# Optimization experiments

Hardware: AMD Instinct MI355X
Metric: run time of the kernel (lower is better)

## Reference

```python
import jax, jax.numpy as jnp
import numpy as np

CN = 64  # cn_base

def conv2d(x, w, b):
    y = jax.lax.conv_general_dilated(x, w, (1, 1), 'SAME', dimension_numbers=('NCHW', 'OIHW', 'NCHW'))
    return y + b[None, :, None, None]

def epipolar_unfold(feat, xy, bw):
    # feat [B,C,h,w], xy [B,np,el,2] int (x,y) -> [B,C,(2bw+1)*el,np]
    B, C, h, w = feat.shape
    npx, el = xy.shape[1], xy.shape[2]
    dy = jnp.arange(-bw, bw + 1)                                   # band offsets [K]
    y = jnp.clip(xy[..., 1][..., None] + dy, 0, h - 1)             # [B,np,el,K]
    x = jnp.clip(xy[..., 0], 0, w - 1)[..., None]                  # [B,np,el,1]
    idx = (y * w + x).reshape(B, -1)                               # [B,np*el*K]
    out = jnp.take_along_axis(feat.reshape(B, C, h * w), idx[:, None, :], axis=2)
    out = out.reshape(B, C, npx, el * (2 * bw + 1))
    return jnp.transpose(out, (0, 1, 3, 2))                        # [B,C,nsz,np]

def setup_inputs():
    key = jax.random.key(0)
    ks = jax.random.split(key, 20)
    b, ns, c, h, w, el, D, bw = 1, 4, 3, 64, 64, 8, 8, 1
    npx = h * w
    nsz = (2 * bw + 1) * el
    cn_emb = (ns - 1) * 2 + 3 * CN + 2 + 6  # 206
    rn = lambda i, shp, s=1.0: jax.random.normal(ks[i], shp, jnp.float32) * s
    return {
        'source_views': rn(0, (b, ns, c, h, w)),
        'source_flows': rn(1, (b, ns, ns - 1, 2, h, w)),
        'psvs': rn(2, (b, ns, c, D, h, w)),
        'warped_source_views': rn(3, (b, ns, ns - 1, c, h, w)),
        'source_posemaps': rn(4, (b, ns, 6)),
        'neighbor_xy': jax.random.randint(ks[5], (b, ns, npx, el, 2), 0, w, jnp.int32),
        'spa_code': rn(6, (b, ns, 2, nsz, npx)),
        'ang_code': rn(7, (b, ns, 6, nsz, npx)),
        'band_width': bw,
        'flow_w': rn(8, (CN, (ns - 1) * 2 + c + (ns - 1) * c, 3, 3), 0.02),
        'flow_b': rn(9, (CN,), 0.02),
        'ctx_w': rn(10, (CN, c, 3, 3), 0.02),
        'ctx_b': rn(11, (CN,), 0.02),
        'wnet_w': rn(12, (cn_emb, 1), 0.02),
        'wnet_b': rn(13, (1,), 0.02),
        'cnet_w': rn(14, (cn_emb, 1), 0.02),
        'cnet_b': rn(15, (1,), 0.02),
        'psv_w': rn(16, (CN, 2 * c, 3, 3), 0.02),
        'psv_b': rn(17, (CN,), 0.02),
        'vref_w': rn(18, (c, c + 2 * ns * CN, 3, 3), 0.02),
        'vref_b': rn(19, (c,), 0.02),
    }

def reference(source_views, source_flows, psvs, warped_source_views, source_posemaps,
              neighbor_xy, spa_code, ang_code, band_width,
              flow_w, flow_b, ctx_w, ctx_b, wnet_w, wnet_b, cnet_w, cnet_b,
              psv_w, psv_b, vref_w, vref_b):
    b, ns, c, h, w = source_views.shape
    npx, el = neighbor_xy.shape[2], neighbor_xy.shape[3]
    ps = int(round(npx ** 0.5))
    D = psvs.shape[3]
    bw = int(band_width)
    nsz = (2 * bw + 1) * el
    B = b * ns
    sv = source_views.reshape(B, c, h, w)
    sf = source_flows.reshape(B, (ns - 1) * 2, h, w)
    wv = warped_source_views.reshape(B, (ns - 1) * c, h, w)
    nxy = neighbor_xy.reshape(B, npx, el, 2)
    spa = spa_code.reshape(B, 2, nsz, npx)
    ang = ang_code.reshape(B, 6, nsz, npx)
    # sub-networks (flowRefNet / ctxNet)
    ce = jax.nn.relu(conv2d(jnp.concatenate([sf, sv, wv], axis=1), flow_w, flow_b))  # [B,64,h,w]
    ctx = jax.nn.relu(conv2d(sv, ctx_w, ctx_b))                                      # [B,64,h,w]
    # epipolar gathers -> [B,C,nsz,np]
    sv_u = epipolar_unfold(sv, nxy, bw)
    ctx_u = epipolar_unfold(ctx, nxy, bw)
    ce_u = epipolar_unfold(ce, nxy, bw)
    sf_u = epipolar_unfold(sf, nxy, bw)
    mu = jnp.broadcast_to(jnp.mean(ce_u, axis=2, keepdims=True), ce_u.shape)
    var = jnp.broadcast_to(jnp.var(ce_u, axis=2, keepdims=True, ddof=1), ce_u.shape)
    emb = jnp.concatenate([sf_u, ce_u, mu, var, spa, ang], axis=1)   # [B,206,nsz,np]
    # weightNet: per-pixel softmax weight over neighbor_size
    emb_t = jnp.transpose(emb, (0, 3, 2, 1))                          # [B,np,nsz,206]
    weight = jax.nn.softmax((emb_t @ wnet_w)[..., 0] + wnet_b[0], axis=-1)  # [B,np,nsz]
    w_sg = jax.lax.stop_gradient(weight)
    interp_view = jnp.einsum('bcnp,bpn->bpc', sv_u, weight)           # [B,np,c]
    interp_ctx = jnp.einsum('bknp,bpn->bpk', ctx_u, w_sg)             # [B,np,64]
    interp_emb = jnp.einsum('bknp,bpn->bpk', emb, w_sg)               # [B,np,206]
    # confNet: softmax confidence over sources
    ie = jnp.transpose(interp_emb.reshape(b, ns, npx, -1), (0, 2, 1, 3))  # [b,np,ns,206]
    confs = jax.nn.softmax((ie @ cnet_w)[..., 0] + cnet_b[0], axis=2)     # [b,np,ns]
    iv4 = interp_view.reshape(b, ns, npx, c)
    blended = jnp.einsum('bspc,bps->bpc', iv4, confs)                 # [b,np,c]
    blended_img = jnp.transpose(blended, (0, 2, 1)).reshape(b, c, ps, ps)
    # psvNet: per depth-slice conv then mean over D
    psv_sl = jnp.transpose(psvs, (0, 1, 3, 2, 4, 5)).reshape(b * ns * D, c, ps, ps)
    bexp = jnp.broadcast_to(blended_img[:, None, None], (b, ns, D, c, ps, ps)).reshape(b * ns * D, c, ps, ps)
    psv_feat = jax.nn.relu(conv2d(jnp.concatenate([psv_sl, bexp], axis=1), psv_w, psv_b))
    psv_feat = psv_feat.reshape(b, ns, D, CN, ps, ps).mean(axis=2)    # [b,ns,64,ps,ps]
    ictx = jnp.transpose(interp_ctx.reshape(b, ns, ps, ps, CN), (0, 1, 4, 2, 3)).reshape(b, ns * CN, ps, ps)
    ref_in = jnp.concatenate([blended_img, ictx, psv_feat.reshape(b, ns * CN, ps, ps)], axis=1)
    ref_novel_view = conv2d(ref_in, vref_w, vref_b)                   # [b,3,ps,ps]
    return (ref_novel_view,
            blended_img,
            jnp.transpose(interp_view.reshape(b, ns, ps, ps, c), (0, 1, 4, 2, 3)),
            weight.reshape(b, ns, ps, ps, nsz),
            jnp.transpose(confs, (0, 2, 1)).reshape(b, ns, ps, ps))
```

## Files before the change

### kernel.cpp

```cpp
#include <hip/hip_runtime.h>
#include <hip/hip_bf16.h>


#define NS   4
#define NPX  4096
#define NSZ  24
#define PS   64
#define VINW 520
#define HW   34

#define OFF0 0
#define OFF1 12288
#define OFF2 24576
#define OFF3 73728
#define OFF4 466944

__device__ unsigned g_cc [NS * NPX * 64];
__device__ float2 g_fld[NS * NPX];
__device__ float2 g_sa [NS * NPX * NSZ];
__device__ __align__(16) unsigned short g_vin [NPX * VINW];
__device__ float g_iv  [NS * NPX * 3];
__device__ float g_clg [NS * NPX];
__device__ float g_fwT [162 * 64];
__device__ float g_cwT [27 * 64];
__device__ float g_pwT [54 * 64];
__device__ __align__(16) unsigned short g_vwT [3 * 9 * VINW];

__device__ __forceinline__ int clampi(int v, int lo, int hi) {
    return v < lo ? lo : (v > hi ? hi : v);
}
__device__ __forceinline__ unsigned bf16_bits(float f) {
    unsigned u = __float_as_uint(f);
    return (u + 0x7fffu + ((u >> 16) & 1u)) >> 16;
}
__device__ __forceinline__ float bf16_lo(unsigned v) { return __uint_as_float(v << 16); }
__device__ __forceinline__ float bf16_hi(unsigned v) { return __uint_as_float(v & 0xffff0000u); }
__device__ __forceinline__ float ldbf(const unsigned short* p, int i) {
    return __uint_as_float(((unsigned)p[i]) << 16);
}

__global__ __launch_bounds__(256) void k_prep(
    const float* __restrict__ fw, const float* __restrict__ cw,
    const float* __restrict__ pw, const float* __restrict__ vw,
    const float* __restrict__ spa, const float* __restrict__ ang,
    const float* __restrict__ ww, const float* __restrict__ cnw)
{
    const int i = blockIdx.x * 256 + threadIdx.x;
    const int stride = gridDim.x * 256;
    for (int d = i; d < 162 * 64; d += stride) g_fwT[d] = fw[(d & 63) * 162 + (d >> 6)];
    for (int d = i; d < 27 * 64;  d += stride) g_cwT[d] = cw[(d & 63) * 27  + (d >> 6)];
    for (int d = i; d < 54 * 64;  d += stride) g_pwT[d] = pw[(d & 63) * 54  + (d >> 6)];
    for (int d = i; d < 3 * 9 * VINW; d += stride) {
        const int oc = d / (9 * VINW), rem = d % (9 * VINW);
        const int t = rem / VINW, nch = rem % VINW;
        float v = 0.f;
        if (nch < 256)      v = vw[(oc * 515 + 3 + nch) * 9 + t];
        else if (nch < 512) v = vw[(oc * 515 + 259 + (nch - 256)) * 9 + t];
        else if (nch < 515) v = vw[(oc * 515 + (nch - 512)) * 9 + t];
        g_vwT[d] = (unsigned short)bf16_bits(v);
    }

    {
        const int s = i >> 12, p = i & 4095;
        float2 acc[NSZ];
        #pragma unroll
        for (int n = 0; n < NSZ; ++n) acc[n] = make_float2(0.f, 0.f);
        #pragma unroll
        for (int c = 0; c < 2; ++c) {
            const float a = ww[198 + c], b = cnw[198 + c];
            #pragma unroll
            for (int n = 0; n < NSZ; ++n) {
                const float v = spa[((s * 2 + c) * NSZ + n) * NPX + p];
                acc[n].x += v * a;
                acc[n].y += v * b;
            }
        }
        #pragma unroll
        for (int c = 0; c < 6; ++c) {
            const float a = ww[200 + c], b = cnw[200 + c];
            #pragma unroll
            for (int n = 0; n < NSZ; ++n) {
                const float v = ang[((s * 6 + c) * NSZ + n) * NPX + p];
                acc[n].x += v * a;
                acc[n].y += v * b;
            }
        }
        float2* dst = g_sa + (size_t)(s * NPX + p) * NSZ;
        #pragma unroll
        for (int n = 0; n < NSZ; ++n) dst[n] = acc[n];
    }
}

__global__ __launch_bounds__(256) void k_convs(
    const float* __restrict__ sv, const float* __restrict__ sf, const float* __restrict__ wv,
    const float* __restrict__ flow_b, const float* __restrict__ ctx_b,
    const float* __restrict__ wnet_w, const float* __restrict__ cnet_w)
{
    __shared__ float lds[18 * 3 * HW];
    const int blk = blockIdx.x;
    const int s = blk >> 7, py = (blk & 127) >> 1, half = blk & 1;
    const int tid = threadIdx.x;

    for (int i = tid; i < 18 * 3 * HW; i += 256) {
        const int lc = i % HW;
        const int rr = (i / HW) % 3;
        const int pl = i / (3 * HW);
        const int iy = py + rr - 1;
        const int ix = half * 32 + lc - 1;
        float v = 0.f;
        if ((unsigned)iy < 64u && (unsigned)ix < 64u) {
            const float* src = (pl < 6) ? (sf + (s * 6 + pl) * NPX)
                             : (pl < 9) ? (sv + (s * 3 + (pl - 6)) * NPX)
                                        : (wv + (s * 9 + (pl - 9)) * NPX);
            v = src[iy * 64 + ix];
        }
        lds[i] = v;
    }
    __syncthreads();

    const int oc  = tid & 63;
    const int wid = tid >> 6;
    const int lc0 = wid * 8;

    float acc_ce[8], acc_ctx[8];
    const float fb = flow_b[oc], cb = ctx_b[oc];
    #pragma unroll
    for (int j = 0; j < 8; ++j) { acc_ce[j] = fb; acc_ctx[j] = cb; }

    for (int pl = 0; pl < 18; ++pl) {
        float w[9];
        #pragma unroll
        for (int t = 0; t < 9; ++t) w[t] = g_fwT[(pl * 9 + t) * 64 + oc];
        float wc[9];
        const bool has_ctx = (pl >= 6 && pl < 9);
        if (has_ctx) {
            #pragma unroll
            for (int t = 0; t < 9; ++t) wc[t] = g_cwT[((pl - 6) * 9 + t) * 64 + oc];
        }
        float c0[3], c1[3], c2[3];
        #pragma unroll
        for (int r = 0; r < 3; ++r) {
            c0[r] = lds[(pl * 3 + r) * HW + lc0];
            c1[r] = lds[(pl * 3 + r) * HW + lc0 + 1];
        }
        #pragma unroll
        for (int j = 0; j < 8; ++j) {
            #pragma unroll
            for (int r = 0; r < 3; ++r)
                c2[r] = lds[(pl * 3 + r) * HW + lc0 + j + 2];
            float a = 0.f;
            #pragma unroll
            for (int r = 0; r < 3; ++r)
                a += c0[r] * w[r * 3 + 0] + c1[r] * w[r * 3 + 1] + c2[r] * w[r * 3 + 2];
            acc_ce[j] += a;
            if (has_ctx) {
                float b2 = 0.f;
                #pragma unroll
                for (int r = 0; r < 3; ++r)
                    b2 += c0[r] * wc[r * 3 + 0] + c1[r] * wc[r * 3 + 1] + c2[r] * wc[r * 3 + 2];
                acc_ctx[j] += b2;
            }
            #pragma unroll
            for (int r = 0; r < 3; ++r) { c0[r] = c1[r]; c1[r] = c2[r]; }
        }
    }

    const float Wce = wnet_w[6 + oc], Cce = cnet_w[6 + oc];
    float awsel = 0.f, acsel = 0.f;
    #pragma unroll
    for (int j = 0; j < 8; ++j) {
        const float ce = fmaxf(acc_ce[j], 0.f);
        const float cx = fmaxf(acc_ctx[j], 0.f);
        const int p = py * 64 + half * 32 + wid * 8 + j;
        g_cc[(s * NPX + p) * 64 + oc] = bf16_bits(ce) | (bf16_bits(cx) << 16);
        float gw = ce * Wce, gc = ce * Cce;
        #pragma unroll
        for (int off = 32; off; off >>= 1) {
            gw += __shfl_xor(gw, off, 64);
            gc += __shfl_xor(gc, off, 64);
        }
        awsel = (oc == j) ? gw : awsel;
        acsel = (oc == j) ? gc : acsel;
    }
    if (oc < 8) {
        const int lpx = wid * 8 + oc;
        float fwv = 0.f, fcv = 0.f;
        #pragma unroll
        for (int c = 0; c < 6; ++c) {
            const float v = lds[(c * 3 + 1) * HW + lpx + 1];
            fwv += v * wnet_w[c];
            fcv += v * cnet_w[c];
        }
        g_fld[s * NPX + py * 64 + half * 32 + lpx] = make_float2(awsel + fwv, acsel + fcv);
    }
}

__global__ __launch_bounds__(256) void k_epi(
    const float* __restrict__ sv, const int* __restrict__ nxy,
    const float* __restrict__ wnet_w, const float* __restrict__ wnet_b,
    const float* __restrict__ cnet_w,
    float* __restrict__ out)
{
    const int blk = blockIdx.x;
    const int wid = threadIdx.x >> 6;
    const int l   = threadIdx.x & 63;
    const int s   = (blk & 7) >> 1;
    const int p   = (blk >> 3) * 8 + (blk & 1) * 4 + wid;

    int q[NSZ];
    #pragma unroll
    for (int e = 0; e < 8; ++e) {
        int nx = nxy[((s * NPX + p) * 8 + e) * 2 + 0];
        int ny = nxy[((s * NPX + p) * 8 + e) * 2 + 1];
        nx = clampi(nx, 0, 63);
        #pragma unroll
        for (int k = 0; k < 3; ++k) {
            int y = clampi(ny + k - 1, 0, 63);
            q[e * 3 + k] = y * 64 + nx;
        }
    }

    const unsigned* ccp = g_cc + (size_t)s * NPX * 64;
    unsigned cc[NSZ];
    #pragma unroll
    for (int n = 0; n < NSZ; ++n) cc[n] = ccp[q[n] * 64 + l];

    float mu = 0.f;
    #pragma unroll
    for (int n = 0; n < NSZ; ++n) mu += bf16_lo(cc[n]);
    mu *= (1.f / 24.f);
    float var = 0.f;
    #pragma unroll
    for (int n = 0; n < NSZ; ++n) { const float d = bf16_lo(cc[n]) - mu; var += d * d; }
    var *= (1.f / 23.f);

    float pw = mu * wnet_w[70 + l] + var * wnet_w[134 + l];
    float pc = mu * cnet_w[70 + l] + var * cnet_w[134 + l];
    #pragma unroll
    for (int off = 32; off; off >>= 1) {
        pw += __shfl_xor(pw, off, 64);
        pc += __shfl_xor(pc, off, 64);
    }
    const float base_w = pw, base_c = pc;

    float Aw = 0.f, Ac = 0.f;
    if (l < NSZ) {
        const float2 A = g_fld[s * NPX + q[l]];
        const float2 B = g_sa[(size_t)(s * NPX + p) * NSZ + l];
        Aw = A.x + B.x; Ac = A.y + B.y;
    }

    float logit = (l < NSZ) ? (Aw + base_w + wnet_b[0]) : -1e30f;
    float mx = logit;
    #pragma unroll
    for (int off = 32; off; off >>= 1) mx = fmaxf(mx, __shfl_xor(mx, off, 64));
    float e = (l < NSZ) ? __expf(logit - mx) : 0.f;
    float ssum = e;
    #pragma unroll
    for (int off = 32; off; off >>= 1) ssum += __shfl_xor(ssum, off, 64);
    const float wgt = e / ssum;

    float clp = (l < NSZ) ? (Ac + base_c) * wgt : 0.f;
    #pragma unroll
    for (int off = 32; off; off >>= 1) clp += __shfl_xor(clp, off, 64);
    if (l == 0) g_clg[s * NPX + p] = clp;

    if (l < NSZ) out[OFF3 + (s * NPX + p) * NSZ + l] = wgt;

    float wall[NSZ];
    #pragma unroll
    for (int n = 0; n < NSZ; ++n) wall[n] = __shfl(wgt, n, 64);

    float sc = 0.f;
    #pragma unroll
    for (int n = 0; n < NSZ; ++n) sc += bf16_hi(cc[n]) * wall[n];
    g_vin[p * VINW + s * 64 + l] = (unsigned short)bf16_bits(sc);

    if (l < 3) {
        float svv = 0.f;
        #pragma unroll
        for (int n = 0; n < NSZ; ++n) svv += sv[(s * 3 + l) * NPX + q[n]] * wall[n];
        g_iv[(s * NPX + p) * 3 + l] = svv;
        out[OFF2 + (s * 3 + l) * NPX + p] = svv;
    }
}

__global__ __launch_bounds__(256) void k_psv(
    const float* __restrict__ psvs, const float* __restrict__ psv_b,
    const float* __restrict__ cnet_b, float* __restrict__ out)
{
    __shared__ float lds[27 * 3 * HW];
    const int blk = blockIdx.x;
    const int s = blk >> 7, py = (blk & 127) >> 1, half = blk & 1;
    const int tid = threadIdx.x;

    for (int i = tid; i < 27 * 3 * HW; i += 256) {
        const int lc = i % HW;
        const int rr = (i / HW) % 3;
        const int pl = i / (3 * HW);
        float v = 0.f;
        if (pl < 24) {
            const int iy = py + rr - 1;
            const int ix = half * 32 + lc - 1;
            if ((unsigned)iy < 64u && (unsigned)ix < 64u)
                v = psvs[(s * 24 + pl) * NPX + iy * 64 + ix];
        }
        lds[i] = v;
    }
    __syncthreads();

    if (tid < 3 * HW) {
        const int r = tid / HW, lc = tid % HW;
        const int iy = py + r - 1, ix = half * 32 + lc - 1;
        if ((unsigned)iy < 64u && (unsigned)ix < 64u) {
            const int p = iy * 64 + ix;
            const float cb2 = cnet_b[0];
            float lg[NS];
            #pragma unroll
            for (int ss = 0; ss < NS; ++ss) lg[ss] = g_clg[ss * NPX + p] + cb2;
            float m = lg[0];
            #pragma unroll
            for (int ss = 1; ss < NS; ++ss) m = fmaxf(m, lg[ss]);
            float ssum = 0.f;
            float conf[NS];
            #pragma unroll
            for (int ss = 0; ss < NS; ++ss) { conf[ss] = __expf(lg[ss] - m); ssum += conf[ss]; }
            const float inv = 1.f / ssum;
            #pragma unroll
            for (int ss = 0; ss < NS; ++ss) conf[ss] *= inv;
            float bl[3];
            #pragma unroll
            for (int c = 0; c < 3; ++c) {
                float a = 0.f;
                #pragma unroll
                for (int ss = 0; ss < NS; ++ss)
                    a += g_iv[(ss * NPX + p) * 3 + c] * conf[ss];
                bl[c] = a;
                lds[((24 + c) * 3 + r) * HW + lc] = a;
            }
            if (s == 0 && r == 1 && lc >= 1 && lc <= 32) {
                #pragma unroll
                for (int ss = 0; ss < NS; ++ss) out[OFF4 + ss * NPX + p] = conf[ss];
                #pragma unroll
                for (int c = 0; c < 3; ++c) {
                    out[OFF1 + c * NPX + p] = bl[c];
                    g_vin[p * VINW + 512 + c] = (unsigned short)bf16_bits(bl[c]);
                }
            }
        }
    }
    __syncthreads();

    const int oc  = tid & 63;
    const int wid = tid >> 6;
    const int lc0 = wid * 8;
    const float bias = psv_b[oc];

    float wp[3][9];
    #pragma unroll
    for (int ic = 0; ic < 3; ++ic)
        #pragma unroll
        for (int t = 0; t < 9; ++t) wp[ic][t] = g_pwT[(ic * 9 + t) * 64 + oc];

    float bconst[8];
    #pragma unroll
    for (int j = 0; j < 8; ++j) bconst[j] = bias;
    for (int ic = 0; ic < 3; ++ic) {
        float w[9];
        #pragma unroll
        for (int t = 0; t < 9; ++t) w[t] = g_pwT[((3 + ic) * 9 + t) * 64 + oc];
        const int pl = 24 + ic;
        float c0[3], c1[3], c2[3];
        #pragma unroll
        for (int r = 0; r < 3; ++r) {
            c0[r] = lds[(pl * 3 + r) * HW + lc0];
            c1[r] = lds[(pl * 3 + r) * HW + lc0 + 1];
        }
        #pragma unroll
        for (int j = 0; j < 8; ++j) {
            #pragma unroll
            for (int r = 0; r < 3; ++r)
                c2[r] = lds[(pl * 3 + r) * HW + lc0 + j + 2];
            float a = 0.f;
            #pragma unroll
            for (int r = 0; r < 3; ++r)
                a += c0[r] * w[r * 3 + 0] + c1[r] * w[r * 3 + 1] + c2[r] * w[r * 3 + 2];
            bconst[j] += a;
            #pragma unroll
            for (int r = 0; r < 3; ++r) { c0[r] = c1[r]; c1[r] = c2[r]; }
        }
    }

    float acc[8];
    #pragma unroll
    for (int j = 0; j < 8; ++j) acc[j] = 0.f;

    for (int d = 0; d < 8; ++d) {
        float a[8];
        #pragma unroll
        for (int j = 0; j < 8; ++j) a[j] = bconst[j];
        #pragma unroll
        for (int ic = 0; ic < 3; ++ic) {
            const int pl = ic * 8 + d;
            float c0[3], c1[3], c2[3];
            #pragma unroll
            for (int r = 0; r < 3; ++r) {
                c0[r] = lds[(pl * 3 + r) * HW + lc0];
                c1[r] = lds[(pl * 3 + r) * HW + lc0 + 1];
            }
            #pragma unroll
            for (int j = 0; j < 8; ++j) {
                #pragma unroll
                for (int r = 0; r < 3; ++r)
                    c2[r] = lds[(pl * 3 + r) * HW + lc0 + j + 2];
                float t2 = 0.f;
                #pragma unroll
                for (int r = 0; r < 3; ++r)
                    t2 += c0[r] * wp[ic][r * 3 + 0] + c1[r] * wp[ic][r * 3 + 1] + c2[r] * wp[ic][r * 3 + 2];
                a[j] += t2;
                #pragma unroll
                for (int r = 0; r < 3; ++r) { c0[r] = c1[r]; c1[r] = c2[r]; }
            }
        }
        #pragma unroll
        for (int j = 0; j < 8; ++j) acc[j] += fmaxf(a[j], 0.f);
    }
    #pragma unroll
    for (int j = 0; j < 8; ++j)
        g_vin[(py * 64 + half * 32 + wid * 8 + j) * VINW + 256 + s * 64 + oc] =
            (unsigned short)bf16_bits(acc[j] * 0.125f);
}

__global__ __launch_bounds__(64) void k_vref(
    const float* __restrict__ vref_b, float* __restrict__ out)
{
    const int p = blockIdx.x;
    const int py = p >> 6, px = p & 63;
    const int l = threadIdx.x;

    float acc[3] = {0.f, 0.f, 0.f};
    #pragma unroll
    for (int t = 0; t < 9; ++t) {
        const int iy = py + t / 3 - 1, ix = px + t % 3 - 1;
        if ((unsigned)iy >= 64u || (unsigned)ix >= 64u) continue;
        const int rowbase = (iy * 64 + ix) * VINW;
        const uint4 vv = *(const uint4*)(g_vin + rowbase + 8 * l);
        float v[8];
        v[0] = bf16_lo(vv.x); v[1] = bf16_hi(vv.x);
        v[2] = bf16_lo(vv.y); v[3] = bf16_hi(vv.y);
        v[4] = bf16_lo(vv.z); v[5] = bf16_hi(vv.z);
        v[6] = bf16_lo(vv.w); v[7] = bf16_hi(vv.w);
        #pragma unroll
        for (int oc = 0; oc < 3; ++oc) {
            const uint4 ww = *(const uint4*)(g_vwT + (oc * 9 + t) * VINW + 8 * l);
            acc[oc] += v[0] * bf16_lo(ww.x) + v[1] * bf16_hi(ww.x)
                     + v[2] * bf16_lo(ww.y) + v[3] * bf16_hi(ww.y)
                     + v[4] * bf16_lo(ww.z) + v[5] * bf16_hi(ww.z)
                     + v[6] * bf16_lo(ww.w) + v[7] * bf16_hi(ww.w);
        }
        if (l < 3) {
            const float bv = ldbf(g_vin, rowbase + 512 + l);
            #pragma unroll
            for (int oc = 0; oc < 3; ++oc)
                acc[oc] += bv * ldbf(g_vwT, (oc * 9 + t) * VINW + 512 + l);
        }
    }
    #pragma unroll
    for (int off = 32; off; off >>= 1) {
        #pragma unroll
        for (int oc = 0; oc < 3; ++oc)
            acc[oc] += __shfl_xor(acc[oc], off, 64);
    }
    if (l == 0) {
        #pragma unroll
        for (int oc = 0; oc < 3; ++oc)
            out[OFF0 + oc * NPX + p] = acc[oc] + vref_b[oc];
    }
}

extern "C" void kernel_launch(void* const* d_in, const int* in_sizes, int n_in,
                              void* d_out, int out_size, void* d_ws, size_t ws_size,
                              hipStream_t stream)
{
    auto find1 = [&](int sz, int fb) -> int {
        for (int i = 0; i < n_in; ++i) if (in_sizes[i] == sz) return i;
        return fb;
    };
    const int i_sv  = find1(49152, 0);
    const int i_sf  = find1(98304, 1);
    const int i_psv = find1(393216, 2);
    const int i_wv  = find1(147456, 3);
    const int i_nxy = find1(262144, 5);
    const int i_spa = find1(786432, 6);
    const int i_ang = find1(2359296, 7);
    const int i_fw  = find1(10368, 9);
    const int i_cw  = find1(1728, 11);
    const int i_pw  = find1(3456, 17);
    const int i_vw  = find1(13905, 19);
    const int i_vb  = find1(3, 20);
    int i_ww = -1, i_cnw = -1;
    for (int i = 0; i < n_in; ++i)
        if (in_sizes[i] == 206) { if (i_ww < 0) i_ww = i; else { i_cnw = i; break; } }
    if (i_ww  < 0) i_ww  = 13;
    if (i_cnw < 0) i_cnw = 15;
    int b64[3] = {10, 12, 18}; int c64 = 0;
    for (int i = 0; i < n_in && c64 < 3; ++i) if (in_sizes[i] == 64) b64[c64++] = i;
    const int i_fb = b64[0], i_cb = b64[1], i_pb = b64[2];
    int i_wb = -1, i_cnb = -1;
    for (int i = i_fw + 1; i < n_in; ++i)
        if (in_sizes[i] == 1) { if (i_wb < 0) i_wb = i; else { i_cnb = i; break; } }
    if (i_wb  < 0) i_wb  = 14;
    if (i_cnb < 0) i_cnb = 16;

    const float* sv     = (const float*)d_in[i_sv];
    const float* sf     = (const float*)d_in[i_sf];
    const float* psvs   = (const float*)d_in[i_psv];
    const float* wv     = (const float*)d_in[i_wv];
    const int*   nxy    = (const int*)d_in[i_nxy];
    const float* spa    = (const float*)d_in[i_spa];
    const float* ang    = (const float*)d_in[i_ang];
    const float* flow_w = (const float*)d_in[i_fw];
    const float* flow_b = (const float*)d_in[i_fb];
    const float* ctx_w  = (const float*)d_in[i_cw];
    const float* ctx_b  = (const float*)d_in[i_cb];
    const float* wnet_w = (const float*)d_in[i_ww];
    const float* wnet_b = (const float*)d_in[i_wb];
    const float* cnet_w = (const float*)d_in[i_cnw];
    const float* cnet_b = (const float*)d_in[i_cnb];
    const float* psv_w  = (const float*)d_in[i_pw];
    const float* psv_b  = (const float*)d_in[i_pb];
    const float* vref_w = (const float*)d_in[i_vw];
    const float* vref_b = (const float*)d_in[i_vb];
    (void)d_ws; (void)ws_size; (void)out_size;

    float* out = (float*)d_out;

    k_prep <<<64, 256, 0, stream>>>(flow_w, ctx_w, psv_w, vref_w, spa, ang, wnet_w, cnet_w);
    k_convs<<<512, 256, 0, stream>>>(sv, sf, wv, flow_b, ctx_b, wnet_w, cnet_w);
    k_epi  <<<4096, 256, 0, stream>>>(sv, nxy, wnet_w, wnet_b, cnet_w, out);
    k_psv  <<<512, 256, 0, stream>>>(psvs, psv_b, cnet_b, out);
    k_vref <<<4096, 64, 0, stream>>>(vref_b, out);
}
```

Before: 177.3 us.

## Fuse five stage kernels into one cooperative persistent kernel with grid syncs

```diff
diff --git a/kernel.cpp b/kernel.cpp
--- a/kernel.cpp
+++ b/kernel.cpp
@@ -1,5 +1,8 @@
 #include <hip/hip_runtime.h>
 #include <hip/hip_bf16.h>
+#include <hip/hip_cooperative_groups.h>
+
+namespace cg = cooperative_groups;
 
 
 #define NS   4
@@ -39,48 +42,52 @@
     return __uint_as_float(((unsigned)p[i]) << 16);
 }
 
-__global__ __launch_bounds__(256) void k_prep(
-    const float* __restrict__ fw, const float* __restrict__ cw,
-    const float* __restrict__ pw, const float* __restrict__ vw,
-    const float* __restrict__ spa, const float* __restrict__ ang,
-    const float* __restrict__ ww, const float* __restrict__ cnw)
-{
-    const int i = blockIdx.x * 256 + threadIdx.x;
-    const int stride = gridDim.x * 256;
-    for (int d = i; d < 162 * 64; d += stride) g_fwT[d] = fw[(d & 63) * 162 + (d >> 6)];
-    for (int d = i; d < 27 * 64;  d += stride) g_cwT[d] = cw[(d & 63) * 27  + (d >> 6)];
-    for (int d = i; d < 54 * 64;  d += stride) g_pwT[d] = pw[(d & 63) * 54  + (d >> 6)];
+struct Params {
+    const float *sv, *sf, *psvs, *wv;
+    const int   *nxy;
+    const float *spa, *ang;
+    const float *fw, *fb, *cw, *cb;
+    const float *ww, *wb, *cnw, *cnb;
+    const float *pw, *pb, *vw, *vb;
+    float *out;
+};
+
+
+__device__ __forceinline__ void prep_body(const Params& P, int i, int stride)
+{
+    for (int d = i; d < 162 * 64; d += stride) g_fwT[d] = P.fw[(d & 63) * 162 + (d >> 6)];
+    for (int d = i; d < 27 * 64;  d += stride) g_cwT[d] = P.cw[(d & 63) * 27  + (d >> 6)];
+    for (int d = i; d < 54 * 64;  d += stride) g_pwT[d] = P.pw[(d & 63) * 54  + (d >> 6)];
     for (int d = i; d < 3 * 9 * VINW; d += stride) {
         const int oc = d / (9 * VINW), rem = d % (9 * VINW);
         const int t = rem / VINW, nch = rem % VINW;
         float v = 0.f;
-        if (nch < 256)      v = vw[(oc * 515 + 3 + nch) * 9 + t];
-        else if (nch < 512) v = vw[(oc * 515 + 259 + (nch - 256)) * 9 + t];
-        else if (nch < 515) v = vw[(oc * 515 + (nch - 512)) * 9 + t];
+        if (nch < 256)      v = P.vw[(oc * 515 + 3 + nch) * 9 + t];
+        else if (nch < 512) v = P.vw[(oc * 515 + 259 + (nch - 256)) * 9 + t];
+        else if (nch < 515) v = P.vw[(oc * 515 + (nch - 512)) * 9 + t];
         g_vwT[d] = (unsigned short)bf16_bits(v);
     }
-
-    {
-        const int s = i >> 12, p = i & 4095;
+    for (int d = i; d < NS * NPX; d += stride) {
+        const int s = d >> 12, p = d & 4095;
         float2 acc[NSZ];
         #pragma unroll
         for (int n = 0; n < NSZ; ++n) acc[n] = make_float2(0.f, 0.f);
         #pragma unroll
         for (int c = 0; c < 2; ++c) {
-            const float a = ww[198 + c], b = cnw[198 + c];
+            const float a = P.ww[198 + c], b = P.cnw[198 + c];
             #pragma unroll
             for (int n = 0; n < NSZ; ++n) {
-                const float v = spa[((s * 2 + c) * NSZ + n) * NPX + p];
+                const float v = P.spa[((s * 2 + c) * NSZ + n) * NPX + p];
                 acc[n].x += v * a;
                 acc[n].y += v * b;
             }
         }
         #pragma unroll
         for (int c = 0; c < 6; ++c) {
-            const float a = ww[200 + c], b = cnw[200 + c];
+            const float a = P.ww[200 + c], b = P.cnw[200 + c];
             #pragma unroll
             for (int n = 0; n < NSZ; ++n) {
-                const float v = ang[((s * 6 + c) * NSZ + n) * NPX + p];
+                const float v = P.ang[((s * 6 + c) * NSZ + n) * NPX + p];
                 acc[n].x += v * a;
                 acc[n].y += v * b;
             }
@@ -91,15 +98,9 @@
     }
 }
 
-__global__ __launch_bounds__(256) void k_convs(
-    const float* __restrict__ sv, const float* __restrict__ sf, const float* __restrict__ wv,
-    const float* __restrict__ flow_b, const float* __restrict__ ctx_b,
-    const float* __restrict__ wnet_w, const float* __restrict__ cnet_w)
-{
-    __shared__ float lds[18 * 3 * HW];
-    const int blk = blockIdx.x;
-    const int s = blk >> 7, py = (blk & 127) >> 1, half = blk & 1;
-    const int tid = threadIdx.x;
+__device__ __forceinline__ void convs_body(const Params& P, float* lds, int b2, int tid)
+{
+    const int s = b2 >> 7, py = (b2 & 127) >> 1, half = b2 & 1;
 
     for (int i = tid; i < 18 * 3 * HW; i += 256) {
         const int lc = i % HW;
@@ -109,9 +110,9 @@
         const int ix = half * 32 + lc - 1;
         float v = 0.f;
         if ((unsigned)iy < 64u && (unsigned)ix < 64u) {
-            const float* src = (pl < 6) ? (sf + (s * 6 + pl) * NPX)
-                             : (pl < 9) ? (sv + (s * 3 + (pl - 6)) * NPX)
-                                        : (wv + (s * 9 + (pl - 9)) * NPX);
+            const float* src = (pl < 6) ? (P.sf + (s * 6 + pl) * NPX)
+                             : (pl < 9) ? (P.sv + (s * 3 + (pl - 6)) * NPX)
+                                        : (P.wv + (s * 9 + (pl - 9)) * NPX);
             v = src[iy * 64 + ix];
         }
         lds[i] = v;
@@ -123,7 +124,7 @@
     const int lc0 = wid * 8;
 
     float acc_ce[8], acc_ctx[8];
-    const float fb = flow_b[oc], cb = ctx_b[oc];
+    const float fb = P.fb[oc], cb = P.cb[oc];
     #pragma unroll
     for (int j = 0; j < 8; ++j) { acc_ce[j] = fb; acc_ctx[j] = cb; }
 
@@ -154,18 +155,18 @@
                 a += c0[r] * w[r * 3 + 0] + c1[r] * w[r * 3 + 1] + c2[r] * w[r * 3 + 2];
             acc_ce[j] += a;
             if (has_ctx) {
-                float b2 = 0.f;
+                float b2f = 0.f;
                 #pragma unroll
                 for (int r = 0; r < 3; ++r)
-                    b2 += c0[r] * wc[r * 3 + 0] + c1[r] * wc[r * 3 + 1] + c2[r] * wc[r * 3 + 2];
-                acc_ctx[j] += b2;
+                    b2f += c0[r] * wc[r * 3 + 0] + c1[r] * wc[r * 3 + 1] + c2[r] * wc[r * 3 + 2];
+                acc_ctx[j] += b2f;
             }
             #pragma unroll
             for (int r = 0; r < 3; ++r) { c0[r] = c1[r]; c1[r] = c2[r]; }
         }
     }
 
-    const float Wce = wnet_w[6 + oc], Cce = cnet_w[6 + oc];
+    const float Wce = P.ww[6 + oc], Cce = P.cnw[6 + oc];
     float awsel = 0.f, acsel = 0.f;
     #pragma unroll
     for (int j = 0; j < 8; ++j) {
@@ -188,30 +189,20 @@
         #pragma unroll
         for (int c = 0; c < 6; ++c) {
             const float v = lds[(c * 3 + 1) * HW + lpx + 1];
-            fwv += v * wnet_w[c];
-            fcv += v * cnet_w[c];
+            fwv += v * P.ww[c];
+            fcv += v * P.cnw[c];
         }
         g_fld[s * NPX + py * 64 + half * 32 + lpx] = make_float2(awsel + fwv, acsel + fcv);
     }
 }
 
-__global__ __launch_bounds__(256) void k_epi(
-    const float* __restrict__ sv, const int* __restrict__ nxy,
-    const float* __restrict__ wnet_w, const float* __restrict__ wnet_b,
-    const float* __restrict__ cnet_w,
-    float* __restrict__ out)
-{
-    const int blk = blockIdx.x;
-    const int wid = threadIdx.x >> 6;
-    const int l   = threadIdx.x & 63;
-    const int s   = (blk & 7) >> 1;
-    const int p   = (blk >> 3) * 8 + (blk & 1) * 4 + wid;
-
+__device__ __forceinline__ void epi_body(const Params& P, int s, int p, int l)
+{
     int q[NSZ];
     #pragma unroll
     for (int e = 0; e < 8; ++e) {
-        int nx = nxy[((s * NPX + p) * 8 + e) * 2 + 0];
-        int ny = nxy[((s * NPX + p) * 8 + e) * 2 + 1];
+        int nx = P.nxy[((s * NPX + p) * 8 + e) * 2 + 0];
+        int ny = P.nxy[((s * NPX + p) * 8 + e) * 2 + 1];
         nx = clampi(nx, 0, 63);
         #pragma unroll
         for (int k = 0; k < 3; ++k) {
@@ -234,8 +225,8 @@
     for (int n = 0; n < NSZ; ++n) { const float d = bf16_lo(cc[n]) - mu; var += d * d; }
     var *= (1.f / 23.f);
 
-    float pw = mu * wnet_w[70 + l] + var * wnet_w[134 + l];
-    float pc = mu * cnet_w[70 + l] + var * cnet_w[134 + l];
+    float pw = mu * P.ww[70 + l] + var * P.ww[134 + l];
+    float pc = mu * P.cnw[70 + l] + var * P.cnw[134 + l];
     #pragma unroll
     for (int off = 32; off; off >>= 1) {
         pw += __shfl_xor(pw, off, 64);
@@ -250,7 +241,7 @@
         Aw = A.x + B.x; Ac = A.y + B.y;
     }
 
-    float logit = (l < NSZ) ? (Aw + base_w + wnet_b[0]) : -1e30f;
+    float logit = (l < NSZ) ? (Aw + base_w + P.wb[0]) : -1e30f;
     float mx = logit;
     #pragma unroll
     for (int off = 32; off; off >>= 1) mx = fmaxf(mx, __shfl_xor(mx, off, 64));
@@ -265,7 +256,7 @@
     for (int off = 32; off; off >>= 1) clp += __shfl_xor(clp, off, 64);
     if (l == 0) g_clg[s * NPX + p] = clp;
 
-    if (l < NSZ) out[OFF3 + (s * NPX + p) * NSZ + l] = wgt;
+    if (l < NSZ) P.out[OFF3 + (s * NPX + p) * NSZ + l] = wgt;
 
     float wall[NSZ];
     #pragma unroll
@@ -279,20 +270,15 @@
     if (l < 3) {
         float svv = 0.f;
         #pragma unroll
-        for (int n = 0; n < NSZ; ++n) svv += sv[(s * 3 + l) * NPX + q[n]] * wall[n];
+        for (int n = 0; n < NSZ; ++n) svv += P.sv[(s * 3 + l) * NPX + q[n]] * wall[n];
         g_iv[(s * NPX + p) * 3 + l] = svv;
-        out[OFF2 + (s * 3 + l) * NPX + p] = svv;
-    }
-}
-
-__global__ __launch_bounds__(256) void k_psv(
-    const float* __restrict__ psvs, const float* __restrict__ psv_b,
-    const float* __restrict__ cnet_b, float* __restrict__ out)
-{
-    __shared__ float lds[27 * 3 * HW];
-    const int blk = blockIdx.x;
-    const int s = blk >> 7, py = (blk & 127) >> 1, half = blk & 1;
-    const int tid = threadIdx.x;
+        P.out[OFF2 + (s * 3 + l) * NPX + p] = svv;
+    }
+}
+
+__device__ __forceinline__ void psv_body(const Params& P, float* lds, int b2, int tid)
+{
+    const int s = b2 >> 7, py = (b2 & 127) >> 1, half = b2 & 1;
 
     for (int i = tid; i < 27 * 3 * HW; i += 256) {
         const int lc = i % HW;
@@ -303,7 +289,7 @@
             const int iy = py + rr - 1;
             const int ix = half * 32 + lc - 1;
             if ((unsigned)iy < 64u && (unsigned)ix < 64u)
-                v = psvs[(s * 24 + pl) * NPX + iy * 64 + ix];
+                v = P.psvs[(s * 24 + pl) * NPX + iy * 64 + ix];
         }
         lds[i] = v;
     }
@@ -314,7 +300,7 @@
         const int iy = py + r - 1, ix = half * 32 + lc - 1;
         if ((unsigned)iy < 64u && (unsigned)ix < 64u) {
             const int p = iy * 64 + ix;
-            const float cb2 = cnet_b[0];
+            const float cb2 = P.cnb[0];
             float lg[NS];
             #pragma unroll
             for (int ss = 0; ss < NS; ++ss) lg[ss] = g_clg[ss * NPX + p] + cb2;
@@ -340,10 +326,10 @@
             }
             if (s == 0 && r == 1 && lc >= 1 && lc <= 32) {
                 #pragma unroll
-                for (int ss = 0; ss < NS; ++ss) out[OFF4 + ss * NPX + p] = conf[ss];
+                for (int ss = 0; ss < NS; ++ss) P.out[OFF4 + ss * NPX + p] = conf[ss];
                 #pragma unroll
                 for (int c = 0; c < 3; ++c) {
-                    out[OFF1 + c * NPX + p] = bl[c];
+                    P.out[OFF1 + c * NPX + p] = bl[c];
                     g_vin[p * VINW + 512 + c] = (unsigned short)bf16_bits(bl[c]);
                 }
             }
@@ -354,7 +340,7 @@
     const int oc  = tid & 63;
     const int wid = tid >> 6;
     const int lc0 = wid * 8;
-    const float bias = psv_b[oc];
+    const float bias = P.pb[oc];
 
     float wp[3][9];
     #pragma unroll
@@ -431,13 +417,9 @@
             (unsigned short)bf16_bits(acc[j] * 0.125f);
 }
 
-__global__ __launch_bounds__(64) void k_vref(
-    const float* __restrict__ vref_b, float* __restrict__ out)
-{
-    const int p = blockIdx.x;
+__device__ __forceinline__ void vref_body(const Params& P, int p, int l)
+{
     const int py = p >> 6, px = p & 63;
-    const int l = threadIdx.x;
-
     float acc[3] = {0.f, 0.f, 0.f};
     #pragma unroll
     for (int t = 0; t < 9; ++t) {
@@ -474,8 +456,86 @@
     if (l == 0) {
         #pragma unroll
         for (int oc = 0; oc < 3; ++oc)
-            out[OFF0 + oc * NPX + p] = acc[oc] + vref_b[oc];
-    }
+            P.out[OFF0 + oc * NPX + p] = acc[oc] + P.vb[oc];
+    }
+}
+
+__global__ __launch_bounds__(256, 1) void k_all(Params P)
+{
+    cg::grid_group grid = cg::this_grid();
+    __shared__ float lds[27 * 3 * HW];
+
+    const int b   = blockIdx.x;
+    const int tid = threadIdx.x;
+    const int l   = tid & 63;
+    const int wid = tid >> 6;
+
+    prep_body(P, b * 256 + tid, 256 * 256);
+    grid.sync();
+
+    #pragma unroll
+    for (int u = 0; u < 2; ++u) {
+        convs_body(P, lds, b * 2 + u, tid);
+        __syncthreads();
+    }
+    grid.sync();
+
+    {
+        const int bs = b & 7, hi = b >> 3;
+        const int s = bs >> 1, parity = bs & 1;
+        for (int it = 0; it < 16; ++it) {
+            const int p = (hi * 16 + it) * 8 + parity * 4 + wid;
+            epi_body(P, s, p, l);
+        }
+    }
+    grid.sync();
+
+    #pragma unroll
+    for (int u = 0; u < 2; ++u) {
+        psv_body(P, lds, b * 2 + u, tid);
+        __syncthreads();
+    }
+    grid.sync();
+
+    {
+        const int wg = b * 4 + wid;
+        #pragma unroll
+        for (int j = 0; j < 4; ++j)
+            vref_body(P, wg * 4 + j, l);
+    }
+}
+
+
+__global__ __launch_bounds__(256) void k_prep(Params P)
+{
+    prep_body(P, blockIdx.x * 256 + threadIdx.x, gridDim.x * 256);
+}
+
+__global__ __launch_bounds__(256) void k_convs(Params P)
+{
+    __shared__ float lds[18 * 3 * HW];
+    convs_body(P, lds, blockIdx.x, threadIdx.x);
+}
+
+__global__ __launch_bounds__(256) void k_epi(Params P)
+{
+    const int blk = blockIdx.x;
+    const int wid = threadIdx.x >> 6;
+    const int l   = threadIdx.x & 63;
+    const int s   = (blk & 7) >> 1;
+    const int p   = (blk >> 3) * 8 + (blk & 1) * 4 + wid;
+    epi_body(P, s, p, l);
+}
+
+__global__ __launch_bounds__(256) void k_psv(Params P)
+{
+    __shared__ float lds[27 * 3 * HW];
+    psv_body(P, lds, blockIdx.x, threadIdx.x);
+}
+
+__global__ __launch_bounds__(64) void k_vref(Params P)
+{
+    vref_body(P, blockIdx.x, threadIdx.x);
 }
 
 extern "C" void kernel_launch(void* const* d_in, const int* in_sizes, int n_in,
@@ -512,32 +572,37 @@
     if (i_wb  < 0) i_wb  = 14;
     if (i_cnb < 0) i_cnb = 16;
 
-    const float* sv     = (const float*)d_in[i_sv];
-    const float* sf     = (const float*)d_in[i_sf];
-    const float* psvs   = (const float*)d_in[i_psv];
-    const float* wv     = (const float*)d_in[i_wv];
-    const int*   nxy    = (const int*)d_in[i_nxy];
-    const float* spa    = (const float*)d_in[i_spa];
-    const float* ang    = (const float*)d_in[i_ang];
-    const float* flow_w = (const float*)d_in[i_fw];
-    const float* flow_b = (const float*)d_in[i_fb];
-    const float* ctx_w  = (const float*)d_in[i_cw];
-    const float* ctx_b  = (const float*)d_in[i_cb];
-    const float* wnet_w = (const float*)d_in[i_ww];
-    const float* wnet_b = (const float*)d_in[i_wb];
-    const float* cnet_w = (const float*)d_in[i_cnw];
-    const float* cnet_b = (const float*)d_in[i_cnb];
-    const float* psv_w  = (const float*)d_in[i_pw];
-    const float* psv_b  = (const float*)d_in[i_pb];
-    const float* vref_w = (const float*)d_in[i_vw];
-    const float* vref_b = (const float*)d_in[i_vb];
+    Params P;
+    P.sv   = (const float*)d_in[i_sv];
+    P.sf   = (const float*)d_in[i_sf];
+    P.psvs = (const float*)d_in[i_psv];
+    P.wv   = (const float*)d_in[i_wv];
+    P.nxy  = (const int*)d_in[i_nxy];
+    P.spa  = (const float*)d_in[i_spa];
+    P.ang  = (const float*)d_in[i_ang];
+    P.fw   = (const float*)d_in[i_fw];
+    P.fb   = (const float*)d_in[i_fb];
+    P.cw   = (const float*)d_in[i_cw];
+    P.cb   = (const float*)d_in[i_cb];
+    P.ww   = (const float*)d_in[i_ww];
+    P.wb   = (const float*)d_in[i_wb];
+    P.cnw  = (const float*)d_in[i_cnw];
+    P.cnb  = (const float*)d_in[i_cnb];
+    P.pw   = (const float*)d_in[i_pw];
+    P.pb   = (const float*)d_in[i_pb];
+    P.vw   = (const float*)d_in[i_vw];
+    P.vb   = (const float*)d_in[i_vb];
+    P.out  = (float*)d_out;
     (void)d_ws; (void)ws_size; (void)out_size;
 
-    float* out = (float*)d_out;
-
-    k_prep <<<64, 256, 0, stream>>>(flow_w, ctx_w, psv_w, vref_w, spa, ang, wnet_w, cnet_w);
-    k_convs<<<512, 256, 0, stream>>>(sv, sf, wv, flow_b, ctx_b, wnet_w, cnet_w);
-    k_epi  <<<4096, 256, 0, stream>>>(sv, nxy, wnet_w, wnet_b, cnet_w, out);
-    k_psv  <<<512, 256, 0, stream>>>(psvs, psv_b, cnet_b, out);
-    k_vref <<<4096, 64, 0, stream>>>(vref_b, out);
-}
+    void* args[] = { &P };
+    hipError_t err = hipLaunchCooperativeKernel((void*)k_all, dim3(256), dim3(256),
+                                                args, 0, stream);
+    if (err != hipSuccess) {
+        k_prep <<<64, 256, 0, stream>>>(P);
+        k_convs<<<512, 256, 0, stream>>>(P);
+        k_epi  <<<4096, 256, 0, stream>>>(P);
+        k_psv  <<<512, 256, 0, stream>>>(P);
+        k_vref <<<4096, 64, 0, stream>>>(P);
+    }
+}
```

New measurement: 387.4 us. 2.19x slower.
